# Kernel optimization log

Hardware: AMD Instinct MI355X
Metric: run time of the kernel (lower is better)

## Reference

```python
import jax, jax.numpy as jnp
import numpy as np

N = 10000   # nodes
E = 100000  # edges
B = 64      # graphs
HID = 128


def setup_inputs() -> dict:
    key = jax.random.key(0)
    ks = iter(jax.random.split(key, 64))
    def nrm(shape, s=0.1):
        return jax.random.normal(next(ks), shape, dtype=jnp.float32) * s
    inp = {}
    inp["x"] = nrm((N, 1), 1.0)
    inp["node_type"] = jax.random.randint(next(ks), (N,), 0, 2)
    inp["edge_index"] = jax.random.randint(next(ks), (2, E), 0, N)
    inp["edge_attr"] = nrm((E, 1), 1.0)
    inp["batch"] = jnp.sort(jax.random.randint(next(ks), (N,), 0, B))
    inp["vp_w"] = nrm((1, HID)); inp["vp_b"] = nrm((HID,))
    inp["type_emb"] = nrm((2, HID))
    def conv(pre, fin, h, c):
        inp[pre + "_wl"] = nrm((fin, h * c)); inp[pre + "_bl"] = nrm((h * c,))
        inp[pre + "_wr"] = nrm((fin, h * c)); inp[pre + "_br"] = nrm((h * c,))
        inp[pre + "_we"] = nrm((1, h * c));  inp[pre + "_att"] = nrm((h, c))
        inp[pre + "_bias"] = nrm((h * c if pre != "c3" else c,))
    conv("c1", HID, 8, HID)
    conv("c2", HID * 8, 2, HID)
    conv("c3", HID * 2, 1, HID)
    inp["m1_w"] = nrm((HID, HID)); inp["m1_b"] = nrm((HID,))
    inp["ln1_g"] = jnp.ones((HID,), jnp.float32); inp["ln1_b"] = jnp.zeros((HID,), jnp.float32)
    inp["m2_w"] = nrm((HID, HID // 2)); inp["m2_b"] = nrm((HID // 2,))
    inp["ln2_g"] = jnp.ones((HID // 2,), jnp.float32); inp["ln2_b"] = jnp.zeros((HID // 2,), jnp.float32)
    inp["m3_w"] = nrm((HID // 2, 1)); inp["m3_b"] = nrm((1,))
    return inp


def _gatv2(x, src, dst, ea, wl, bl, wr, br, we, att, bias, heads, out_ch, concat):
    """PyG GATv2Conv (eval mode): add self-loops (edge_attr fill='mean' over dst),
    attn = (att * leaky_relu(Wl x_src + Wr x_dst + We e)).sum(-1), segment-softmax
    over destination, scatter-add of alpha * Wl x_src."""
    n = x.shape[0]
    ones = jnp.ones((ea.shape[0], 1), ea.dtype)
    deg = jax.ops.segment_sum(ones, dst, num_segments=n)
    loop_attr = jax.ops.segment_sum(ea, dst, num_segments=n) / jnp.maximum(deg, 1.0)
    ar = jnp.arange(n, dtype=src.dtype)
    src2 = jnp.concatenate([src, ar])
    dst2 = jnp.concatenate([dst, ar])
    ea2 = jnp.concatenate([ea, loop_attr], axis=0)
    xl = (x @ wl + bl).reshape(n, heads, out_ch)   # source transform
    xr = (x @ wr + br).reshape(n, heads, out_ch)   # target transform
    e = (ea2 @ we).reshape(-1, heads, out_ch)      # [E2, H, C]
    msg = xl[src2]                                 # [E2, H, C]
    z = jax.nn.leaky_relu(msg + xr[dst2] + e, 0.2)
    score = jnp.einsum('ehc,hc->eh', z, att)       # [E2, H]
    smax = jax.ops.segment_max(score, dst2, num_segments=n)
    ex = jnp.exp(score - smax[dst2])
    denom = jax.ops.segment_sum(ex, dst2, num_segments=n)
    alpha = ex / denom[dst2]
    out = jax.ops.segment_sum(alpha[:, :, None] * msg, dst2, num_segments=n)
    out = out.reshape(n, heads * out_ch) if concat else out.mean(axis=1)
    return out + bias


def _layernorm(v, g, b):
    mu = v.mean(-1, keepdims=True)
    var = v.var(-1, keepdims=True)
    return (v - mu) / jnp.sqrt(var + 1e-5) * g + b


def reference(x, node_type, edge_index, edge_attr, batch,
              vp_w, vp_b, type_emb,
              c1_wl, c1_bl, c1_wr, c1_br, c1_we, c1_att, c1_bias,
              c2_wl, c2_bl, c2_wr, c2_br, c2_we, c2_att, c2_bias,
              c3_wl, c3_bl, c3_wr, c3_br, c3_we, c3_att, c3_bias,
              m1_w, m1_b, ln1_g, ln1_b, m2_w, m2_b, ln2_g, ln2_b, m3_w, m3_b):
    src, dst = edge_index[0], edge_index[1]
    h = x @ vp_w + vp_b + type_emb[node_type]
    h = jax.nn.leaky_relu(_gatv2(h, src, dst, edge_attr, c1_wl, c1_bl, c1_wr, c1_br, c1_we, c1_att, c1_bias, 8, HID, True), 0.2)
    h = jax.nn.leaky_relu(_gatv2(h, src, dst, edge_attr, c2_wl, c2_bl, c2_wr, c2_br, c2_we, c2_att, c2_bias, 2, HID, True), 0.2)
    h = jax.nn.leaky_relu(_gatv2(h, src, dst, edge_attr, c3_wl, c3_bl, c3_wr, c3_br, c3_we, c3_att, c3_bias, 1, HID, False), 0.2)
    # masked global mean pool over node_type == 0
    w = (node_type == 0).astype(h.dtype)
    sums = jax.ops.segment_sum(h * w[:, None], batch, num_segments=B)
    cnts = jax.ops.segment_sum(w, batch, num_segments=B)
    pooled = sums / jnp.maximum(cnts, 1.0)[:, None]
    h1 = jax.nn.leaky_relu(_layernorm(pooled @ m1_w + m1_b, ln1_g, ln1_b), 0.2)
    h2 = jax.nn.leaky_relu(_layernorm(h1 @ m2_w + m2_b, ln2_g, ln2_b), 0.2)
    return (h2 @ m3_w + m3_b).squeeze(-1)
```

## Files before the change

kernel.cpp:

```cpp
#include <hip/hip_runtime.h>
#include <math.h>

#define NN 10000
#define NE 100000
#define NBATCH 64

typedef short bf16x8 __attribute__((ext_vector_type(8)));
typedef float f32x4 __attribute__((ext_vector_type(4)));

__device__ __forceinline__ float lrelu(float v){ return fmaxf(v, 0.2f*v); }

__device__ __forceinline__ unsigned short f2bf(float x){
  unsigned int u = __float_as_uint(x);
  u += 0x7fffu + ((u >> 16) & 1u);
  return (unsigned short)(u >> 16);
}
__device__ __forceinline__ float bf2f(unsigned short u){
  return __uint_as_float(((unsigned int)u) << 16);
}

__global__ __launch_bounds__(256) void prep_kernel(
    const float* __restrict__ vp_w, const float* __restrict__ vp_b,
    const float* __restrict__ type_emb,
    const float* __restrict__ c1_wl, const float* __restrict__ c1_bl,
    const float* __restrict__ c1_wr, const float* __restrict__ c1_br,
    float* __restrict__ Ul, float* __restrict__ CTl,
    float* __restrict__ Ur, float* __restrict__ CTr,
    const float* __restrict__ c2_wl, const float* __restrict__ c2_wr,
    const float* __restrict__ c3_wl, const float* __restrict__ c3_wr,
    unsigned short* __restrict__ W2lT, unsigned short* __restrict__ W2rT,
    unsigned short* __restrict__ W3lT, unsigned short* __restrict__ W3rT,
    float* __restrict__ zbase, int zero_words)
{
  __shared__ float t[64][65];
  int b = blockIdx.x;
  int tid = threadIdx.x;
  if (b < 144){
    const float* in; unsigned short* out; int K, N, idx;
    if (b < 64)      { in=c2_wl; out=W2lT; K=1024; N=256; idx=b; }
    else if (b <128) { in=c2_wr; out=W2rT; K=1024; N=256; idx=b-64; }
    else if (b <136) { in=c3_wl; out=W3lT; K=256;  N=128; idx=b-128; }
    else             { in=c3_wr; out=W3rT; K=256;  N=128; idx=b-136; }
    int K64 = K >> 6;
    int kx = idx % K64, nx = idx / K64;
    int k0 = kx*64, n0 = nx*64;
    int lr = tid >> 4;
    int lc = (tid & 15) * 4;
#pragma unroll
    for (int i=0;i<4;++i){
      int r = lr + i*16;
      float4 v = *(const float4*)(in + (size_t)(k0+r)*N + n0 + lc);
      t[r][lc+0]=v.x; t[r][lc+1]=v.y; t[r][lc+2]=v.z; t[r][lc+3]=v.w;
    }
    __syncthreads();
    int sr = tid >> 3;
    int sc = (tid & 7) * 8;
#pragma unroll
    for (int i=0;i<2;++i){
      int n = sr + i*32;
      unsigned short tmp[8];
#pragma unroll
      for (int j=0;j<8;++j) tmp[j] = f2bf(t[sc+j][n]);
      unsigned short* op = out + (size_t)(n0+n)*K + k0 + sc;
      *(ushort4*)op       = make_ushort4(tmp[0],tmp[1],tmp[2],tmp[3]);
      *(ushort4*)(op + 4) = make_ushort4(tmp[4],tmp[5],tmp[6],tmp[7]);
    }
  } else if (b < 148){
    int j = (b-144)*256 + tid;
    float ul=0.f, c0l=0.f, c1l=0.f, ur=0.f, c0r=0.f, c1r=0.f;
    for (int k=0; k<128; ++k){
      float a = c1_wl[k*1024 + j], bb = c1_wr[k*1024 + j];
      float vw = vp_w[k], vb = vp_b[k], t0 = type_emb[k], t1 = type_emb[128+k];
      ul += vw*a; ur += vw*bb;
      c0l += (vb+t0)*a; c1l += (vb+t1)*a;
      c0r += (vb+t0)*bb; c1r += (vb+t1)*bb;
    }
    float bl = c1_bl[j], br = c1_br[j];
    Ul[j]=ul; Ur[j]=ur;
    CTl[j]      = c0l + bl;
    CTl[1024+j] = c1l + bl;
    CTr[j]      = c0r + br;
    CTr[1024+j] = c1r + br;
  } else {
    for (int i = (b-148)*256 + tid; i < zero_words; i += 32*256)
      zbase[i] = 0.f;
  }
}

__global__ void count_kernel(const int* __restrict__ dst, const float* __restrict__ ea,
                             int* __restrict__ deg, float* __restrict__ loop_sum){
  int e = blockIdx.x*256 + threadIdx.x;
  if (e < NE){
    int d = dst[e];
    atomicAdd(&deg[d], 1);
    atomicAdd(&loop_sum[d], ea[e]);
  }
}

__global__ __launch_bounds__(1024) void scan_kernel(const int* __restrict__ deg,
    const float* __restrict__ loop_sum, const float* __restrict__ x,
    const int* __restrict__ ntype,
    int* __restrict__ rowptr, float* __restrict__ loop_attr, float2* __restrict__ xt){
  __shared__ int wtot[16];
  int tid = threadIdx.x;
  int lane = tid & 63, wid = tid >> 6;
  int base = tid*10;
  int d[10]; int run = 0;
#pragma unroll
  for (int j=0;j<10;++j){
    int i = base + j;
    int v = (i < NN) ? deg[i] : 0;
    run += v; d[j] = run;
  }
  int T = run;
  int incl = T;
#pragma unroll
  for (int off=1; off<64; off<<=1){
    int s = __shfl_up(incl, off, 64);
    if (lane >= off) incl += s;
  }
  if (lane == 63) wtot[wid] = incl;
  __syncthreads();
  int wpre = 0;
  for (int w2=0; w2<wid; ++w2) wpre += wtot[w2];
  int ebase = wpre + incl - T;
#pragma unroll
  for (int j=0;j<10;++j){
    int i = base + j;
    if (i < NN){
      int v = d[j] - ((j==0) ? 0 : d[j-1]);
      rowptr[i] = ebase + d[j] - v;
      loop_attr[i] = loop_sum[i] / fmaxf((float)v, 1.f);
      xt[i] = make_float2(x[i], (float)ntype[i]);
    }
  }
  if (tid == 1023) rowptr[NN] = wpre + incl;
}

__global__ void fill_kernel(const int* __restrict__ src, const int* __restrict__ dst,
                            const float* __restrict__ ea, const int* __restrict__ rowptr,
                            int* __restrict__ rowctr, int2* __restrict__ se){
  int e = blockIdx.x*256 + threadIdx.x;
  if (e < NE){
    int d = dst[e];
    int p = rowptr[d] + atomicAdd(&rowctr[d], 1);
    se[p] = make_int2(src[e], __float_as_int(ea[e]));
  }
}

__global__ __launch_bounds__(256) void conv1_fused(
    const int* __restrict__ rowptr, const int2* __restrict__ se,
    const float* __restrict__ loop_attr, const float2* __restrict__ xt,
    const float* __restrict__ Ul, const float* __restrict__ Ur,
    const float* __restrict__ CTl, const float* __restrict__ CTr,
    const float* __restrict__ we, const float* __restrict__ att,
    const float* __restrict__ bias, unsigned short* __restrict__ out)
{
  int n = blockIdx.x*4 + (threadIdx.x >> 6);
  if (n >= NN) return;
  int lane = threadIdx.x & 63;
  int h = lane >> 3, sub = lane & 7;
  int ch0 = h*128 + sub*16;
  float ul[16], wev[16], atv[16], cn0[16], cnd[16];
#pragma unroll
  for (int v=0; v<16; ++v){ ul[v]=Ul[ch0+v]; wev[v]=we[ch0+v]; atv[v]=att[ch0+v]; }
  int beg = rowptr[n], deg = rowptr[n+1]-beg;
  float2 xtn = xt[n];
  float xn = xtn.x, tfn = xtn.y;
  float la = loop_attr[n];
  const float* ctr = (tfn != 0.f) ? (CTr+1024) : CTr;
#pragma unroll
  for (int v=0; v<16; ++v){
    float c0 = CTl[ch0+v], c1 = CTl[1024+ch0+v];
    cn0[v] = fmaf(xn, Ur[ch0+v], ctr[ch0+v]) + c0;
    cnd[v] = c1 - c0;
  }
  const int2* sp = se + beg;
  float l = 0.f, s1 = 0.f, st1 = 0.f;
  int s; float ea;
  if (deg > 0){ int2 q = sp[0]; s = q.x; ea = __int_as_float(q.y); }
  else        { s = n; ea = la; }
  float2 xc = xt[s];
  for (int idx=0; idx<=deg; ++idx){
    int nx = idx+1;
    int2 qn;
    if (nx < deg) qn = sp[nx];
    else          qn = make_int2(n, __float_as_int(la));
    float2 xnx = xt[qn.x];
    float xs = xc.x, tf = xc.y;
    float acc = 0.f;
#pragma unroll
    for (int v=0; v<16; ++v){
      float t = fmaf(tf, cnd[v], cn0[v]);
      float z = fmaf(xs, ul[v], fmaf(ea, wev[v], t));
      acc = fmaf(atv[v], fmaxf(z, 0.2f*z), acc);
    }
    acc += __shfl_xor(acc, 1, 8);
    acc += __shfl_xor(acc, 2, 8);
    acc += __shfl_xor(acc, 4, 8);
    float pe = __expf(acc);
    l += pe;
    s1  = fmaf(pe, xs, s1);
    st1 = fmaf(pe, tf, st1);
    ea = __int_as_float(qn.y); xc = xnx;
  }
  float inv = 1.f/l;
  s1 *= inv;
  float s21 = st1 * inv;
  float s20 = 1.f - s21;
  bf16x8 w0v, w1v;
#pragma unroll
  for (int v=0; v<16; ++v){
    float c0 = CTl[ch0+v], c1 = CTl[1024+ch0+v];
    float o = lrelu(fmaf(s1, ul[v], fmaf(s20, c0, fmaf(s21, c1, bias[ch0+v]))));
    if (v < 8) w0v[v]   = (short)f2bf(o);
    else       w1v[v-8] = (short)f2bf(o);
  }
  unsigned short* op = out + (size_t)n*1024 + ch0;
  *(bf16x8*)op       = w0v;
  *(bf16x8*)(op + 8) = w1v;
}

template<int H, int NPB, int VPT, bool ONLY0, bool OUTBF, bool INBF>
__global__ __launch_bounds__(64*NPB) void conv_kernel(
    const int* __restrict__ rowptr, const int2* __restrict__ se,
    const float* __restrict__ loop_attr, const int* __restrict__ ntype,
    const void* __restrict__ Xv, int stride, int xr_off,
    const float* __restrict__ we, const float* __restrict__ att, const float* __restrict__ bias,
    void* __restrict__ out)
{
  const int HC = 64*VPT;
  const int TPH = 64/H;
  int n = blockIdx.x*NPB + (threadIdx.x >> 6);
  if (n >= NN) return;
  if (ONLY0 && ntype[n] != 0) return;
  int tid = threadIdx.x & 63;
  int ch0 = tid * VPT;
  const float* Xf = (const float*)Xv;
  const unsigned short* Xb = (const unsigned short*)Xv;
  float wev[VPT], atv[VPT], biv[VPT], xrv[VPT];
#pragma unroll
  for (int v=0; v<VPT; ++v){
    int ch = ch0+v;
    wev[v]=we[ch]; atv[v]=att[ch]; biv[v]=bias[ch];
  }
  if constexpr (INBF){
    ushort4 q = *(const ushort4*)(Xb + (size_t)n*stride + xr_off + ch0);
    xrv[0]=bf2f(q.x); xrv[1]=bf2f(q.y); xrv[2]=bf2f(q.z); xrv[3]=bf2f(q.w);
  } else {
#pragma unroll
    for (int v=0; v<VPT; ++v) xrv[v]=Xf[(size_t)n*stride + xr_off + ch0+v];
  }
  float ls[4], A[4][VPT];
#pragma unroll
  for (int k=0; k<4; ++k){
    ls[k] = 0.f;
#pragma unroll
    for (int v=0; v<VPT; ++v) A[k][v] = 0.f;
  }
  int beg=rowptr[n], end=rowptr[n+1];
  float la = loop_attr[n];
  for (int j=beg; j<=end; j+=4){
    bool val[4]; int sx[4]; float ex[4];
#pragma unroll
    for (int k=0; k<4; ++k){
      int pos = j + k;
      val[k] = pos <= end;
      int2 q;
      if (pos < end) q = se[pos];
      else           q = make_int2(n, __float_as_int(la));
      sx[k] = q.x; ex[k] = __int_as_float(q.y);
    }
    float xv[4][VPT];
#pragma unroll
    for (int k=0; k<4; ++k){
      if constexpr (INBF){
        ushort4 q = *(const ushort4*)(Xb + (size_t)sx[k]*stride + ch0);
        xv[k][0]=bf2f(q.x); xv[k][1]=bf2f(q.y); xv[k][2]=bf2f(q.z); xv[k][3]=bf2f(q.w);
      } else if constexpr (VPT == 4){
        float4 q = *(const float4*)(Xf + (size_t)sx[k]*stride + ch0);
        xv[k][0]=q.x; xv[k][1]=q.y; xv[k][2]=q.z; xv[k][3]=q.w;
      } else {
        float2 q = *(const float2*)(Xf + (size_t)sx[k]*stride + ch0);
        xv[k][0]=q.x; xv[k][1]=q.y;
      }
    }
    float p[4];
#pragma unroll
    for (int k=0; k<4; ++k){
      float acc = 0.f;
#pragma unroll
      for (int v=0; v<VPT; ++v)
        acc += atv[v]*lrelu(xv[k][v]+xrv[v]+ex[k]*wev[v]);
      p[k] = acc;
    }
#pragma unroll
    for (int mm=1; mm<TPH; mm<<=1){
#pragma unroll
      for (int k=0; k<4; ++k) p[k] += __shfl_xor(p[k], mm, 64);
    }
#pragma unroll
    for (int k=0; k<4; ++k){
      float pe = val[k] ? __expf(p[k]) : 0.f;
      ls[k] += pe;
#pragma unroll
      for (int v=0; v<VPT; ++v) A[k][v] = fmaf(pe, xv[k][v], A[k][v]);
    }
  }
  float lt = (ls[0]+ls[1]) + (ls[2]+ls[3]);
  float inv = 1.f/lt;
  size_t baseo=(size_t)n*HC+ch0;
  if constexpr (OUTBF){
    unsigned short* ob = (unsigned short*)out;
    ushort4 o;
    o.x = f2bf(lrelu(((A[0][0]+A[1][0])+(A[2][0]+A[3][0]))*inv+biv[0]));
    o.y = f2bf(lrelu(((A[0][1]+A[1][1])+(A[2][1]+A[3][1]))*inv+biv[1]));
    o.z = f2bf(lrelu(((A[0][2]+A[1][2])+(A[2][2]+A[3][2]))*inv+biv[2]));
    o.w = f2bf(lrelu(((A[0][3]+A[1][3])+(A[2][3]+A[3][3]))*inv+biv[3]));
    *(ushort4*)(ob + baseo) = o;
  } else {
    float* of = (float*)out;
#pragma unroll
    for (int v=0; v<VPT; ++v)
      of[baseo+v] = lrelu(((A[0][v]+A[1][v])+(A[2][v]+A[3][v]))*inv+biv[v]);
  }
}

template<bool OUTBF>
__global__ __launch_bounds__(256) void gemm_dual_lds(
    const short* __restrict__ Abf,
    const short* __restrict__ WlT, const short* __restrict__ WrT,
    const float* __restrict__ bl, const float* __restrict__ br,
    void* __restrict__ Out, int M, int K, int NcH, int cgrid, int rgrid)
{
  __shared__ short lds[12288];
  int id = blockIdx.x;
  int xcd = id & 7, slot = id >> 3;
  int nb = slot % cgrid;
  int rowgroup = (slot / cgrid) * 8 + xcd;
  if (rowgroup >= rgrid) return;
  int row0 = rowgroup * 128;
  int NC2 = 2*NcH;
  int halfx = NcH >> 6;
  int isR = nb >= halfx;
  const short* WT = isR ? WrT : WlT;
  const float* bias = isR ? br : bl;
  int col0 = (nb - (isR ? halfx : 0)) * 64;
  int gcol0 = nb * 64;
  int tid = threadIdx.x;
  int lane = tid & 63, wave = tid >> 6;
  int wm = wave >> 1, wn = wave & 1;
  int quad = lane >> 4, l16 = lane & 15;

  const short* asrc[4];
#pragma unroll
  for (int i=0;i<4;++i){
    int c = wave*256 + i*64 + lane;
    int m = c >> 3, j = c & 7;
    int gr = row0 + m; gr = gr < M ? gr : M-1;
    asrc[i] = Abf + (size_t)gr*K + ((j ^ (m & 7)) << 3);
  }
  const short* bsrc[2];
#pragma unroll
  for (int i=0;i<2;++i){
    int c = wave*128 + i*64 + lane;
    int nloc = c >> 3, j = c & 7;
    bsrc[i] = WT + (size_t)(col0 + nloc)*K + ((j ^ (nloc & 7)) << 3);
  }

  float biasv[2] = { bias[col0 + wn*32 + l16], bias[col0 + wn*32 + 16 + l16] };
  f32x4 acc[4][2];
#pragma unroll
  for (int f=0; f<4; ++f)
#pragma unroll
    for (int g=0; g<2; ++g) acc[f][g] = (f32x4){0.f,0.f,0.f,0.f};

  int niter = K >> 6;
  for (int it=0; it<niter; ++it){
    int k0 = it << 6;
#pragma unroll
    for (int i=0;i<4;++i)
      __builtin_amdgcn_global_load_lds(asrc[i] + k0, &lds[(wave*256 + i*64)*8], 16, 0, 0);
#pragma unroll
    for (int i=0;i<2;++i)
      __builtin_amdgcn_global_load_lds(bsrc[i] + k0, &lds[8192 + (wave*128 + i*64)*8], 16, 0, 0);
    __syncthreads();
#pragma unroll
    for (int s=0; s<2; ++s){
      int t = s*4 + quad;
      bf16x8 af[4], bfv[2];
#pragma unroll
      for (int f=0; f<4; ++f){
        int m = wm*64 + f*16 + l16;
        af[f] = *(const bf16x8*)&lds[m*64 + ((t ^ (m & 7)) << 3)];
      }
#pragma unroll
      for (int g=0; g<2; ++g){
        int nloc = wn*32 + g*16 + l16;
        bfv[g] = *(const bf16x8*)&lds[8192 + nloc*64 + ((t ^ (nloc & 7)) << 3)];
      }
#pragma unroll
      for (int f=0; f<4; ++f)
#pragma unroll
        for (int g=0; g<2; ++g)
          acc[f][g] = __builtin_amdgcn_mfma_f32_16x16x32_bf16(af[f], bfv[g], acc[f][g], 0,0,0);
    }
    __syncthreads();
  }

#pragma unroll
  for (int f=0; f<4; ++f){
    int rbase = row0 + wm*64 + f*16 + quad*4;
#pragma unroll
    for (int r=0; r<4; ++r){
      int rr = rbase + r;
      if (rr < M){
#pragma unroll
        for (int g=0; g<2; ++g){
          int cc = gcol0 + wn*32 + g*16 + l16;
          float val = acc[f][g][r] + biasv[g];
          if constexpr (OUTBF) ((unsigned short*)Out)[(size_t)rr*NC2 + cc] = f2bf(val);
          else                 ((float*)Out)[(size_t)rr*NC2 + cc] = val;
        }
      }
    }
  }
}

__device__ __forceinline__ int lbound(const int* __restrict__ a, int n, int key){
  int lo = 0, hi = n;
  while (lo < hi){ int mid = (lo+hi) >> 1; if (a[mid] < key) lo = mid+1; else hi = mid; }
  return lo;
}

__global__ __launch_bounds__(128) void head_kernel(
    const float* __restrict__ h3, const int* __restrict__ ntype, const int* __restrict__ batch,
    const float* __restrict__ m1w, const float* __restrict__ m1b,
    const float* __restrict__ g1, const float* __restrict__ b1,
    const float* __restrict__ m2w, const float* __restrict__ m2b,
    const float* __restrict__ g2, const float* __restrict__ b2,
    const float* __restrict__ m3w, const float* __restrict__ m3b,
    float* __restrict__ out)
{
  __shared__ float p[128];
  __shared__ float hb[128];
  __shared__ float red[128];
  int b = blockIdx.x, j = threadIdx.x;
  int lo = lbound(batch, NN, b);
  int hi = lbound(batch, NN, b+1);
  float s = 0.f, cnt = 0.f;
  int n = lo;
  for (; n + 3 < hi; n += 4){
    float w0 = (ntype[n]   == 0) ? 1.f : 0.f;
    float w1 = (ntype[n+1] == 0) ? 1.f : 0.f;
    float w2 = (ntype[n+2] == 0) ? 1.f : 0.f;
    float w3 = (ntype[n+3] == 0) ? 1.f : 0.f;
    s += w0*h3[(size_t)n*128 + j]     + w1*h3[(size_t)(n+1)*128 + j]
       + w2*h3[(size_t)(n+2)*128 + j] + w3*h3[(size_t)(n+3)*128 + j];
    cnt += w0 + w1 + w2 + w3;
  }
  for (; n < hi; ++n){
    float w = (ntype[n] == 0) ? 1.f : 0.f;
    s += w*h3[(size_t)n*128 + j];
    cnt += w;
  }
  p[j] = s / fmaxf(cnt, 1.f);
  __syncthreads();
  float a = m1b[j];
  for (int k=0; k<128; ++k) a += p[k]*m1w[k*128 + j];
  red[j] = a; __syncthreads();
  for (int off=64; off>0; off>>=1){ if (j<off) red[j] += red[j+off]; __syncthreads(); }
  float mu = red[0] * (1.f/128.f);
  __syncthreads();
  float d = a - mu;
  red[j] = d*d; __syncthreads();
  for (int off=64; off>0; off>>=1){ if (j<off) red[j] += red[j+off]; __syncthreads(); }
  float var = red[0] * (1.f/128.f);
  __syncthreads();
  hb[j] = lrelu(d * rsqrtf(var + 1e-5f) * g1[j] + b1[j]);
  __syncthreads();
  float a2 = 0.f;
  if (j < 64){
    a2 = m2b[j];
    for (int k=0; k<128; ++k) a2 += hb[k]*m2w[k*64 + j];
  }
  red[j] = (j<64) ? a2 : 0.f; __syncthreads();
  for (int off=64; off>0; off>>=1){ if (j<off) red[j] += red[j+off]; __syncthreads(); }
  float mu2 = red[0] * (1.f/64.f);
  __syncthreads();
  float d2 = a2 - mu2;
  red[j] = (j<64) ? d2*d2 : 0.f; __syncthreads();
  for (int off=64; off>0; off>>=1){ if (j<off) red[j] += red[j+off]; __syncthreads(); }
  float var2 = red[0] * (1.f/64.f);
  __syncthreads();
  if (j < 64) hb[j] = lrelu(d2 * rsqrtf(var2 + 1e-5f) * g2[j] + b2[j]);
  __syncthreads();
  if (j == 0){
    float o = m3b[0];
    for (int k=0; k<64; ++k) o += hb[k]*m3w[k];
    out[b] = o;
  }
}

extern "C" void kernel_launch(void* const* d_in, const int* in_sizes, int n_in,
                              void* d_out, int out_size, void* d_ws, size_t ws_size,
                              hipStream_t stream)
{
  const float* x        = (const float*)d_in[0];
  const int*   ntype    = (const int*)d_in[1];
  const int*   ei       = (const int*)d_in[2];
  const float* eattr    = (const float*)d_in[3];
  const int*   batch    = (const int*)d_in[4];
  const float* vp_w     = (const float*)d_in[5];
  const float* vp_b     = (const float*)d_in[6];
  const float* type_emb = (const float*)d_in[7];
  const float* c1_wl = (const float*)d_in[8];  const float* c1_bl = (const float*)d_in[9];
  const float* c1_wr = (const float*)d_in[10]; const float* c1_br = (const float*)d_in[11];
  const float* c1_we = (const float*)d_in[12]; const float* c1_att= (const float*)d_in[13];
  const float* c1_bias=(const float*)d_in[14];
  const float* c2_wl = (const float*)d_in[15]; const float* c2_bl = (const float*)d_in[16];
  const float* c2_wr = (const float*)d_in[17]; const float* c2_br = (const float*)d_in[18];
  const float* c2_we = (const float*)d_in[19]; const float* c2_att= (const float*)d_in[20];
  const float* c2_bias=(const float*)d_in[21];
  const float* c3_wl = (const float*)d_in[22]; const float* c3_bl = (const float*)d_in[23];
  const float* c3_wr = (const float*)d_in[24]; const float* c3_br = (const float*)d_in[25];
  const float* c3_we = (const float*)d_in[26]; const float* c3_att= (const float*)d_in[27];
  const float* c3_bias=(const float*)d_in[28];
  const float* m1_w = (const float*)d_in[29]; const float* m1_b = (const float*)d_in[30];
  const float* ln1_g= (const float*)d_in[31]; const float* ln1_b= (const float*)d_in[32];
  const float* m2_w = (const float*)d_in[33]; const float* m2_b = (const float*)d_in[34];
  const float* ln2_g= (const float*)d_in[35]; const float* ln2_b= (const float*)d_in[36];
  const float* m3_w = (const float*)d_in[37]; const float* m3_b = (const float*)d_in[38];
  const int* esrc = ei;
  const int* edst = ei + NE;
  float* outp = (float*)d_out;
  (void)in_sizes; (void)n_in; (void)out_size; (void)ws_size;

  char* w = (char*)d_ws;
  auto alloc = [&](size_t bytes) -> void* {
    void* p = (void*)w;
    w += (bytes + 255) & ~(size_t)255;
    return p;
  };
  unsigned short* h1bf = (unsigned short*)alloc((size_t)NN*1024*2);
  unsigned short* X2   = (unsigned short*)alloc((size_t)NN*512*2);
  unsigned short* h2bf = (unsigned short*)alloc((size_t)NN*256*2);
  float* X3   = (float*)alloc((size_t)NN*256*4);
  float* h3   = (float*)alloc((size_t)NN*128*4);
  unsigned short* W2lT = (unsigned short*)alloc((size_t)256*1024*2);
  unsigned short* W2rT = (unsigned short*)alloc((size_t)256*1024*2);
  unsigned short* W3lT = (unsigned short*)alloc((size_t)128*256*2);
  unsigned short* W3rT = (unsigned short*)alloc((size_t)128*256*2);
  float* Ul   = (float*)alloc(1024*4);
  float* CTl  = (float*)alloc(2048*4);
  float* Ur   = (float*)alloc(1024*4);
  float* CTr  = (float*)alloc(2048*4);
  const int zero_words = 3*NN;
  float* zbase = (float*)alloc((size_t)zero_words*4);
  int*   deg      = (int*)zbase;
  int*   rowctr   = (int*)(zbase + NN);
  float* loop_sum = zbase + 2*NN;
  float* loop_attr= (float*)alloc((size_t)NN*4);
  float2* xt      = (float2*)alloc((size_t)NN*8);
  int*   rowptr   = (int*)alloc((size_t)(NN+1)*4);
  int2*  se       = (int2*)alloc((size_t)NE*8);

  prep_kernel<<<180, 256, 0, stream>>>(vp_w, vp_b, type_emb,
      c1_wl, c1_bl, c1_wr, c1_br, Ul, CTl, Ur, CTr,
      c2_wl, c2_wr, c3_wl, c3_wr, W2lT, W2rT, W3lT, W3rT,
      zbase, zero_words);
  count_kernel<<<(NE+255)/256, 256, 0, stream>>>(edst, eattr, deg, loop_sum);
  scan_kernel<<<1, 1024, 0, stream>>>(deg, loop_sum, x, ntype, rowptr, loop_attr, xt);
  fill_kernel<<<(NE+255)/256, 256, 0, stream>>>(esrc, edst, eattr, rowptr, rowctr, se);
  conv1_fused<<<NN/4, 256, 0, stream>>>(rowptr, se, loop_attr, xt,
      Ul, Ur, CTl, CTr, c1_we, c1_att, c1_bias, h1bf);
  gemm_dual_lds<true><<<640, 256, 0, stream>>>(
      (const short*)h1bf, (const short*)W2lT, (const short*)W2rT, c2_bl, c2_br,
      (void*)X2, NN, 1024, 256, 8, 79);
  conv_kernel<2,4,4,false,true,true><<<NN/4, 256, 0, stream>>>(rowptr, se, loop_attr, ntype,
      (const void*)X2, 512, 256, c2_we, c2_att, c2_bias, h2bf);
  gemm_dual_lds<false><<<320, 256, 0, stream>>>(
      (const short*)h2bf, (const short*)W3lT, (const short*)W3rT, c3_bl, c3_br,
      (void*)X3, NN, 256, 128, 4, 79);
  conv_kernel<1,4,2,true,false,false><<<NN/4, 256, 0, stream>>>(rowptr, se, loop_attr, ntype,
      (const void*)X3, 256, 128, c3_we, c3_att, c3_bias, h3);
  head_kernel<<<NBATCH, 128, 0, stream>>>(h3, ntype, batch, m1_w, m1_b, ln1_g, ln1_b,
                                          m2_w, m2_b, ln2_g, ln2_b, m3_w, m3_b, outp);
}
```

Measured before the change: 322.0 us.

## Use 128 threads per node in conv1 with 8 channels each and deeper prefetch

The fused first-layer GATv2 kernel now gives each destination node 128 threads handling 8 channels each, instead of 64 threads handling 16. Each head's reduction becomes a 16-lane shuffle, and the grid launches twice as many blocks. The edge loop now prefetches the edge record two steps ahead and the source node's features one step ahead, to hide gather latency. The aim is more parallelism and shorter serial per-edge work on this latency-bound loop, at the cost of duplicated per-edge index and feature loads and an extra shuffle step.

```diff
diff --git a/kernel.cpp b/kernel.cpp
--- a/kernel.cpp
+++ b/kernel.cpp
@@ -156,69 +156,62 @@
     const float* __restrict__ we, const float* __restrict__ att,
     const float* __restrict__ bias, unsigned short* __restrict__ out)
 {
-  int n = blockIdx.x*4 + (threadIdx.x >> 6);
+  int n = blockIdx.x*2 + (threadIdx.x >> 7);
   if (n >= NN) return;
-  int lane = threadIdx.x & 63;
-  int h = lane >> 3, sub = lane & 7;
-  int ch0 = h*128 + sub*16;
-  float ul[16], wev[16], atv[16], cn0[16], cnd[16];
-#pragma unroll
-  for (int v=0; v<16; ++v){ ul[v]=Ul[ch0+v]; wev[v]=we[ch0+v]; atv[v]=att[ch0+v]; }
+  int te = threadIdx.x & 127;
+  int ch0 = te * 8;
+  float ul[8], wev[8], atv[8], cn0[8], cnd[8];
+#pragma unroll
+  for (int v=0; v<8; ++v){ ul[v]=Ul[ch0+v]; wev[v]=we[ch0+v]; atv[v]=att[ch0+v]; }
   int beg = rowptr[n], deg = rowptr[n+1]-beg;
   float2 xtn = xt[n];
-  float xn = xtn.x, tfn = xtn.y;
   float la = loop_attr[n];
-  const float* ctr = (tfn != 0.f) ? (CTr+1024) : CTr;
-#pragma unroll
-  for (int v=0; v<16; ++v){
+  const float* ctr = (xtn.y != 0.f) ? (CTr+1024) : CTr;
+#pragma unroll
+  for (int v=0; v<8; ++v){
     float c0 = CTl[ch0+v], c1 = CTl[1024+ch0+v];
-    cn0[v] = fmaf(xn, Ur[ch0+v], ctr[ch0+v]) + c0;
+    cn0[v] = fmaf(xtn.x, Ur[ch0+v], ctr[ch0+v]) + c0;
     cnd[v] = c1 - c0;
   }
   const int2* sp = se + beg;
+  const int2 self = make_int2(n, __float_as_int(la));
+  int2 qc = (deg > 0) ? sp[0] : self;
+  float2 xc = xt[qc.x];
+  int2 qn = (1 < deg) ? sp[1] : self;
   float l = 0.f, s1 = 0.f, st1 = 0.f;
-  int s; float ea;
-  if (deg > 0){ int2 q = sp[0]; s = q.x; ea = __int_as_float(q.y); }
-  else        { s = n; ea = la; }
-  float2 xc = xt[s];
   for (int idx=0; idx<=deg; ++idx){
-    int nx = idx+1;
-    int2 qn;
-    if (nx < deg) qn = sp[nx];
-    else          qn = make_int2(n, __float_as_int(la));
-    float2 xnx = xt[qn.x];
-    float xs = xc.x, tf = xc.y;
+    int2 qnn = (idx+2 < deg) ? sp[idx+2] : self;
+    float2 xn = xt[qn.x];
+    float xs = xc.x, tf = xc.y, ea = __int_as_float(qc.y);
     float acc = 0.f;
 #pragma unroll
-    for (int v=0; v<16; ++v){
+    for (int v=0; v<8; ++v){
       float t = fmaf(tf, cnd[v], cn0[v]);
       float z = fmaf(xs, ul[v], fmaf(ea, wev[v], t));
       acc = fmaf(atv[v], fmaxf(z, 0.2f*z), acc);
     }
-    acc += __shfl_xor(acc, 1, 8);
-    acc += __shfl_xor(acc, 2, 8);
-    acc += __shfl_xor(acc, 4, 8);
+    acc += __shfl_xor(acc, 1, 16);
+    acc += __shfl_xor(acc, 2, 16);
+    acc += __shfl_xor(acc, 4, 16);
+    acc += __shfl_xor(acc, 8, 16);
     float pe = __expf(acc);
     l += pe;
     s1  = fmaf(pe, xs, s1);
     st1 = fmaf(pe, tf, st1);
-    ea = __int_as_float(qn.y); xc = xnx;
+    qc = qn; xc = xn; qn = qnn;
   }
   float inv = 1.f/l;
   s1 *= inv;
   float s21 = st1 * inv;
   float s20 = 1.f - s21;
-  bf16x8 w0v, w1v;
-#pragma unroll
-  for (int v=0; v<16; ++v){
+  bf16x8 ov;
+#pragma unroll
+  for (int v=0; v<8; ++v){
     float c0 = CTl[ch0+v], c1 = CTl[1024+ch0+v];
     float o = lrelu(fmaf(s1, ul[v], fmaf(s20, c0, fmaf(s21, c1, bias[ch0+v]))));
-    if (v < 8) w0v[v]   = (short)f2bf(o);
-    else       w1v[v-8] = (short)f2bf(o);
-  }
-  unsigned short* op = out + (size_t)n*1024 + ch0;
-  *(bf16x8*)op       = w0v;
-  *(bf16x8*)(op + 8) = w1v;
+    ov[v] = (short)f2bf(o);
+  }
+  *(bf16x8*)(out + (size_t)n*1024 + ch0) = ov;
 }
 
 template<int H, int NPB, int VPT, bool ONLY0, bool OUTBF, bool INBF>
@@ -572,7 +565,7 @@
   count_kernel<<<(NE+255)/256, 256, 0, stream>>>(edst, eattr, deg, loop_sum);
   scan_kernel<<<1, 1024, 0, stream>>>(deg, loop_sum, x, ntype, rowptr, loop_attr, xt);
   fill_kernel<<<(NE+255)/256, 256, 0, stream>>>(esrc, edst, eattr, rowptr, rowctr, se);
-  conv1_fused<<<NN/4, 256, 0, stream>>>(rowptr, se, loop_attr, xt,
+  conv1_fused<<<NN/2, 256, 0, stream>>>(rowptr, se, loop_attr, xt,
       Ul, Ur, CTl, CTr, c1_we, c1_att, c1_bias, h1bf);
   gemm_dual_lds<true><<<640, 256, 0, stream>>>(
       (const short*)h1bf, (const short*)W2lT, (const short*)W2rT, c2_bl, c2_br,
```

Measured after the change: 314.5 us. 2.3% less time.
